# Kernel tuning notes

Hardware: AMD Instinct MI355X
Metric: run time of the kernel (lower is better)

## Reference

```python
import jax, jax.numpy as jnp
import numpy as np

N = 16000        # nodes
E = 256000       # edges
D_IN = 1280      # input node features
HID = 256        # hidden dim (all hidden_dims equal; required by res_linear shapes)
HEADS = 8
C = HID // HEADS # 32 channels per head
G = 32           # graphs in the batch
O = 64           # output labels (GO terms)
NB = 2           # conv blocks = len(hidden_dims) - 1
EPS = 1e-5


def _bn(h, g, b):
    # eval-mode BatchNorm1d with running_mean=0, running_var=1 (init state)
    return h * (g / jnp.sqrt(1.0 + EPS)) + b


def _seg_softmax(logits, seg, num):
    # numerically-stable segment softmax (PyG softmax semantics)
    m = jax.ops.segment_max(logits, seg, num_segments=num)
    e = jnp.exp(logits - m[seg])
    s = jax.ops.segment_sum(e, seg, num_segments=num)
    return e / (s[seg] + 1e-16)


def setup_inputs() -> dict:
    key = jax.random.key(0)
    ks = jax.random.split(key, 16)
    w = lambda i, sh: jax.random.normal(ks[i], sh, jnp.float32) * 0.05
    return {
        "x": jax.random.normal(ks[0], (N, D_IN), jnp.float32),
        "edge_index": jax.random.randint(ks[1], (2, E), 0, N),
        "batch": jnp.sort(jax.random.randint(ks[2], (N,), 0, G)),
        # feature_proj: Linear -> ReLU -> BN
        "fp_W": w(3, (D_IN, HID)), "fp_b": jnp.zeros(HID),
        "fp_g": jnp.ones(HID), "fp_be": jnp.zeros(HID),
        # GATv2Conv per block: lin_l, lin_r, att, out-bias
        "gat_Wl": w(4, (NB, HID, HID)), "gat_bl": jnp.zeros((NB, HID)),
        "gat_Wr": w(5, (NB, HID, HID)), "gat_br": jnp.zeros((NB, HID)),
        "gat_att": w(6, (NB, HEADS, C)), "gat_bias": jnp.zeros((NB, HID)),
        # GINConv MLP: Linear -> ReLU -> BN
        "gin_W": w(7, (NB, HID, HID)), "gin_b": jnp.zeros((NB, HID)),
        "gin_g": jnp.ones((NB, HID)), "gin_be": jnp.zeros((NB, HID)),
        # PyG LayerNorm (graph mode) affine
        "ln_g": jnp.ones((NB, HID)), "ln_b": jnp.zeros((NB, HID)),
        # residual linears
        "res_W": w(8, (NB, HID, HID)), "res_b": jnp.zeros((NB, HID)),
        # GlobalAttention gate MLP
        "pool_W1": w(9, (HID, HID)), "pool_b1": jnp.zeros(HID),
        "pool_W2": w(10, (HID, 1)), "pool_b2": jnp.zeros(1),
        # O label heads (hierarchy=None -> just the MLP), stacked
        "head_W1": w(11, (O, HID, 256)), "head_b1": jnp.zeros((O, 256)),
        "head_g": jnp.ones((O, 256)), "head_be": jnp.zeros((O, 256)),
        "head_W2": w(12, (O, 256)), "head_b2": jnp.zeros(O),
    }


def reference(x, edge_index, batch, fp_W, fp_b, fp_g, fp_be,
              gat_Wl, gat_bl, gat_Wr, gat_br, gat_att, gat_bias,
              gin_W, gin_b, gin_g, gin_be, ln_g, ln_b, res_W, res_b,
              pool_W1, pool_b1, pool_W2, pool_b2,
              head_W1, head_b1, head_g, head_be, head_W2, head_b2):
    n = x.shape[0]
    # feature_proj (eval: dropout = identity)
    h = _bn(jax.nn.relu(x @ fp_W + fp_b), fp_g, fp_be)

    src0, dst0 = edge_index[0], edge_index[1]
    loop = jnp.arange(n)
    src = jnp.concatenate([src0, loop])  # GATv2 adds self-loops by default
    dst = jnp.concatenate([dst0, loop])

    for i in range(NB):
        # ---- GATv2Conv (no activation after, per original control flow) ----
        xl = (h @ gat_Wl[i] + gat_bl[i]).reshape(n, HEADS, C)
        xr = (h @ gat_Wr[i] + gat_br[i]).reshape(n, HEADS, C)
        msg = xl[src]                                   # [E', H, C]
        eact = jax.nn.leaky_relu(msg + xr[dst], 0.2)
        logit = jnp.einsum('ehc,hc->eh', eact, gat_att[i])
        alpha = _seg_softmax(logit, dst, n)             # [E', H]
        h = jax.ops.segment_sum(alpha[:, :, None] * msg, dst,
                                num_segments=n).reshape(n, HID) + gat_bias[i]
        # ---- GINConv: nn((1+0)*x + sum_neighbors), then leaky_relu ----
        agg = jax.ops.segment_sum(h[src0], dst0, num_segments=n)
        gin = _bn(jax.nn.relu((h + agg) @ gin_W[i] + gin_b[i]), gin_g[i], gin_be[i])
        h = jax.nn.leaky_relu(gin, 0.2)
        # ---- PyG LayerNorm (graph mode, batch=None: global mean/std) + residual ----
        mu = h.mean()
        sd = jnp.std(h)
        ln = (h - mu) / (sd + EPS) * ln_g[i] + ln_b[i]
        h = jax.nn.leaky_relu(ln + (h @ res_W[i] + res_b[i]), 0.2)

    # ---- GlobalAttention pooling ----
    gate = jnp.tanh(h @ pool_W1 + pool_b1) @ pool_W2 + pool_b2   # [N, 1]
    a = _seg_softmax(gate[:, 0], batch, G)
    emb = jax.ops.segment_sum(a[:, None] * h, batch, num_segments=G)  # [G, HID]

    # ---- O label heads (hierarchy None -> MLP only), vectorized ----
    z = jnp.einsum('bd,odh->boh', emb, head_W1) + head_b1[None]
    z = _bn(jax.nn.silu(z), head_g[None], head_be[None])
    out = jnp.einsum('boh,oh->bo', z, head_W2) + head_b2[None]
    return out[:, :, None]  # torch.stack(outputs, dim=1) -> [G, O, 1]
```

## Files before the change

### kernel.cpp

```cpp
#include <hip/hip_runtime.h>
#include <math.h>

#define N_NODES 16000
#define N_EDGES 256000
#define EPE (N_EDGES + N_NODES)
#define DIN 1280
#define HID 256
#define HEADS 8
#define CPH 32
#define NG 32
#define NO 64
#define EPSC 1e-5f
#define CAP 32
#define XPAD 264
#define SPAD 40

typedef __bf16 bf16;
typedef __attribute__((ext_vector_type(8))) __bf16 bf16x8;
typedef __attribute__((ext_vector_type(4))) float floatx4;

__device__ __forceinline__ float lrelu(float v) { return v > 0.f ? v : 0.2f * v; }
__device__ __forceinline__ float bflo(unsigned int u) { return __uint_as_float(u << 16); }
__device__ __forceinline__ float bfhi(unsigned int u) { return __uint_as_float(u & 0xffff0000u); }
__device__ __forceinline__ unsigned int bfpack(float x, float y) {
    bf16 b0 = (bf16)x, b1 = (bf16)y;
    return ((unsigned int)*(unsigned short*)&b0) | (((unsigned int)*(unsigned short*)&b1) << 16);
}

__global__ void wconv_gen(const float* __restrict__ W, bf16* __restrict__ Wt, int K, int total) {
    int idx = blockIdx.x * 256 + threadIdx.x;
    if (idx >= total) return;
    int per = K * HID;
    int l = idx / per, rem = idx - l * per;
    int n = rem / K, k = rem - n * K;
    Wt[idx] = (bf16)W[(size_t)l * per + (size_t)k * HID + n];
}

__global__ void wconv_pair(const float* __restrict__ Wl, const float* __restrict__ Wr,
                           bf16* __restrict__ Wt) {
    int idx = blockIdx.x * 256 + threadIdx.x;
    int n = idx >> 8, k = idx & 255;
    float v = (n < 256) ? Wl[(size_t)k * HID + n] : Wr[(size_t)k * HID + (n - 256)];
    Wt[idx] = (bf16)v;
}

__global__ __launch_bounds__(256) void gemm64(
    const bf16* __restrict__ A, const bf16* __restrict__ Bt,
    const float* __restrict__ bias, const float* __restrict__ bias2,
    bf16* __restrict__ C, int K, int ldc, int mode,
    const float* __restrict__ g, const float* __restrict__ be,
    float2* __restrict__ statp, const float* __restrict__ stat)
{
    __shared__ __align__(16) bf16 As[2][64 * SPAD];
    __shared__ __align__(16) bf16 Bs[2][64 * SPAD];
    const int tid = threadIdx.x;
    const int bm = blockIdx.y * 64, bn = blockIdx.x * 64;
    const int w = tid >> 6, lane = tid & 63;
    const int wm = w * 16;
    const int lrow = lane & 15, lk8 = (lane >> 4) * 8;
    const int row = tid >> 2, k8 = (tid & 3) * 8;

    const bf16* gA = A + (size_t)(bm + row) * K + k8;
    const bf16* gB = Bt + (size_t)(bn + row) * K + k8;

    floatx4 acc[4];
#pragma unroll
    for (int j = 0; j < 4; j++) acc[j] = (floatx4){0.f, 0.f, 0.f, 0.f};

    const int nk = K >> 5;
    bf16x8 ra = *(const bf16x8*)gA;
    bf16x8 rb = *(const bf16x8*)gB;

    for (int it = 0; it < nk; ++it) {
        int p = it & 1;
        *(bf16x8*)&As[p][row * SPAD + k8] = ra;
        *(bf16x8*)&Bs[p][row * SPAD + k8] = rb;
        __syncthreads();
        if (it + 1 < nk) {
            ra = *(const bf16x8*)(gA + (it + 1) * 32);
            rb = *(const bf16x8*)(gB + (it + 1) * 32);
        }
        bf16x8 af = *(const bf16x8*)&As[p][(wm + lrow) * SPAD + lk8];
        bf16x8 bfr[4];
#pragma unroll
        for (int j = 0; j < 4; j++) bfr[j] = *(const bf16x8*)&Bs[p][(16 * j + lrow) * SPAD + lk8];
#pragma unroll
        for (int j = 0; j < 4; j++)
            acc[j] = __builtin_amdgcn_mfma_f32_16x16x32_bf16(af, bfr[j], acc[j], 0, 0, 0);
    }

    const float inv = rsqrtf(1.f + EPSC);
    const int row0 = bm + wm + (lane >> 4) * 4;
    float mu = 0.f, rs = 0.f;
    if (mode == 3) {
        const float inv_n = 1.f / (float)((size_t)N_NODES * HID);
        mu = stat[0] * inv_n;
        float var = stat[1] * inv_n - mu * mu;
        rs = 1.f / (sqrtf(fmaxf(var, 0.f)) + EPSC);
    }
    float sz = 0.f, sq = 0.f;
#pragma unroll
    for (int j = 0; j < 4; j++) {
        int col = bn + 16 * j + lrow;
        float bcol = (col < HID) ? bias[col] : bias2[col - HID];
        float gc = (mode >= 2) ? g[col] : 0.f;
        float bec = (mode >= 2) ? be[col] : 0.f;
#pragma unroll
        for (int r = 0; r < 4; r++) {
            float z = acc[j][r] + bcol;
            if (mode == 2) {
                z = fmaxf(z, 0.f) * (gc * inv) + bec;
                z = lrelu(z);
                sz += z; sq += z * z;
            } else if (mode == 3) {
                float h = (float)A[(size_t)(row0 + r) * K + col];
                z = (h - mu) * rs * gc + bec + z;
                z = lrelu(z);
            }
            C[(size_t)(row0 + r) * ldc + col] = (bf16)z;
        }
    }
    if (mode == 2) {
        for (int o = 32; o > 0; o >>= 1) { sz += __shfl_down(sz, o); sq += __shfl_down(sq, o); }
        __syncthreads();
        float* rs_ = (float*)&As[0][0];
        float* rq_ = (float*)&Bs[0][0];
        if (lane == 0) { rs_[w] = sz; rq_[w] = sq; }
        __syncthreads();
        if (tid == 0)
            statp[blockIdx.y * gridDim.x + blockIdx.x] =
                make_float2(rs_[0] + rs_[1] + rs_[2] + rs_[3],
                            rq_[0] + rq_[1] + rq_[2] + rq_[3]);
    }
}

__global__ __launch_bounds__(256, 1) void gemm_f32A(
    const float* __restrict__ A, const bf16* __restrict__ Bt,
    const float* __restrict__ bias, bf16* __restrict__ C, int K,
    const float* __restrict__ g, const float* __restrict__ be)
{
    __shared__ __align__(16) bf16 As[2][128 * SPAD];
    __shared__ __align__(16) bf16 Bs[2][128 * SPAD];
    const int tid = threadIdx.x;
    const int bm = blockIdx.y * 128, bn = blockIdx.x * 128;
    const int w = tid >> 6, lane = tid & 63;
    const int wm = (w & 1) * 64, wn = (w >> 1) * 64;
    const int lrow = lane & 15, lk8 = (lane >> 4) * 8;

    floatx4 acc[4][4];
#pragma unroll
    for (int i = 0; i < 4; i++)
#pragma unroll
        for (int j = 0; j < 4; j++) acc[i][j] = (floatx4){0.f, 0.f, 0.f, 0.f};

    const int r2 = tid >> 1, c2 = tid & 1;
    const float* gA = A + (size_t)(bm + r2) * K + c2 * 16;
    const bf16* gB = Bt + (size_t)(bn + r2) * K + c2 * 16;
    bf16* sA = &As[0][r2 * SPAD + c2 * 16];
    bf16* sB = &Bs[0][r2 * SPAD + c2 * 16];

    const int nk = K >> 5;
    float4 a[4][4];
    bf16x8 b[4][2];
#pragma unroll
    for (int u = 0; u < 4; u++) {
        const float* pa = gA + u * 32;
        a[u][0] = *(const float4*)(pa + 0);
        a[u][1] = *(const float4*)(pa + 4);
        a[u][2] = *(const float4*)(pa + 8);
        a[u][3] = *(const float4*)(pa + 12);
        const bf16* pb = gB + u * 32;
        b[u][0] = *(const bf16x8*)(pb + 0);
        b[u][1] = *(const bf16x8*)(pb + 8);
    }

    for (int it0 = 0; it0 < nk; it0 += 4) {
#pragma unroll
        for (int u = 0; u < 4; u++) {
            const int it = it0 + u;
            const int p = u & 1;
            const int po = p * 128 * SPAD;
            bf16x8 h0, h1;
            h0[0] = (bf16)a[u][0].x; h0[1] = (bf16)a[u][0].y; h0[2] = (bf16)a[u][0].z; h0[3] = (bf16)a[u][0].w;
            h0[4] = (bf16)a[u][1].x; h0[5] = (bf16)a[u][1].y; h0[6] = (bf16)a[u][1].z; h0[7] = (bf16)a[u][1].w;
            h1[0] = (bf16)a[u][2].x; h1[1] = (bf16)a[u][2].y; h1[2] = (bf16)a[u][2].z; h1[3] = (bf16)a[u][2].w;
            h1[4] = (bf16)a[u][3].x; h1[5] = (bf16)a[u][3].y; h1[6] = (bf16)a[u][3].z; h1[7] = (bf16)a[u][3].w;
            *(bf16x8*)(sA + po + 0) = h0;
            *(bf16x8*)(sA + po + 8) = h1;
            *(bf16x8*)(sB + po + 0) = b[u][0];
            *(bf16x8*)(sB + po + 8) = b[u][1];
            __syncthreads();
            if (it + 4 < nk) {
                const float* pa = gA + (it + 4) * 32;
                a[u][0] = *(const float4*)(pa + 0);
                a[u][1] = *(const float4*)(pa + 4);
                a[u][2] = *(const float4*)(pa + 8);
                a[u][3] = *(const float4*)(pa + 12);
                const bf16* pb = gB + (it + 4) * 32;
                b[u][0] = *(const bf16x8*)(pb + 0);
                b[u][1] = *(const bf16x8*)(pb + 8);
            }
            bf16x8 af[4], bfr[4];
#pragma unroll
            for (int i = 0; i < 4; i++) af[i] = *(const bf16x8*)&As[p][(wm + 16 * i + lrow) * SPAD + lk8];
#pragma unroll
            for (int j = 0; j < 4; j++) bfr[j] = *(const bf16x8*)&Bs[p][(wn + 16 * j + lrow) * SPAD + lk8];
#pragma unroll
            for (int i = 0; i < 4; i++)
#pragma unroll
                for (int j = 0; j < 4; j++)
                    acc[i][j] = __builtin_amdgcn_mfma_f32_16x16x32_bf16(af[i], bfr[j], acc[i][j], 0, 0, 0);
        }
    }

    const float inv = rsqrtf(1.f + EPSC);
#pragma unroll
    for (int j = 0; j < 4; j++) {
        int col = bn + wn + 16 * j + lrow;
        float bcol = bias[col];
        float gc = g[col] * inv;
        float bec = be[col];
#pragma unroll
        for (int i = 0; i < 4; i++) {
            int row0 = bm + wm + 16 * i + (lane >> 4) * 4;
#pragma unroll
            for (int r = 0; r < 4; r++) {
                float z = fmaxf(acc[i][j][r] + bcol, 0.f) * gc + bec;
                C[(size_t)(row0 + r) * HID + col] = (bf16)z;
            }
        }
    }
}

__global__ void hist_kernel(const int* __restrict__ ei, int* __restrict__ cnt) {
    int e = blockIdx.x * 256 + threadIdx.x;
    if (e >= EPE) return;
    int d = (e < N_EDGES) ? ei[N_EDGES + e] : (e - N_EDGES);
    atomicAdd(&cnt[d], 1);
}

__global__ __launch_bounds__(1024) void scan_kernel(const int* __restrict__ cnt,
                                                    int* __restrict__ roff, int* __restrict__ cursor,
                                                    const int* __restrict__ batch,
                                                    int* __restrict__ gstart) {
    __shared__ int wsum[16];
    int t = threadIdx.x;
    int base = t * 16;
    int local[16]; int s = 0;
#pragma unroll
    for (int i = 0; i < 16; i++) {
        int idx = base + i;
        int v = (idx < N_NODES) ? cnt[idx] : 0;
        local[i] = s; s += v;
    }
    int lane = t & 63, wid = t >> 6;
    int incl = s;
    for (int o = 1; o < 64; o <<= 1) { int v = __shfl_up(incl, o); if (lane >= o) incl += v; }
    if (lane == 63) wsum[wid] = incl;
    __syncthreads();
    if (t == 0) { int a = 0; for (int k = 0; k < 16; k++) { int v = wsum[k]; wsum[k] = a; a += v; } }
    __syncthreads();
    int texcl = incl - s + wsum[wid];
#pragma unroll
    for (int i = 0; i < 16; i++) {
        int idx = base + i;
        if (idx < N_NODES) { int o = texcl + local[i]; roff[idx] = o; cursor[idx] = o; }
    }
    if (t == 1023) roff[N_NODES] = texcl + s;
    if (t <= NG) {
        int lo = 0, hi = N_NODES;
        while (lo < hi) { int mid = (lo + hi) >> 1; if (batch[mid] < t) lo = mid + 1; else hi = mid; }
        gstart[t] = lo;
    }
}

__global__ void scatter_kernel(const int* __restrict__ ei, int* __restrict__ cursor,
                               int* __restrict__ esrc) {
    int e = blockIdx.x * 256 + threadIdx.x;
    if (e >= EPE) return;
    int s, d;
    if (e < N_EDGES) { s = ei[e]; d = ei[N_EDGES + e]; }
    else { s = d = e - N_EDGES; }
    int pos = atomicAdd(&cursor[d], 1);
    esrc[pos] = s;
}

__global__ __launch_bounds__(256) void gat_fused(
    const bf16* __restrict__ XLR, const int* __restrict__ roff, const int* __restrict__ esrc,
    const float* __restrict__ att, const float* __restrict__ gbias, bf16* __restrict__ out)
{
    const int d = blockIdx.x, t = threadIdx.x;
    const int beg = roff[d], deg = roff[d + 1] - beg;
    __shared__ __align__(16) bf16 xs[CAP][XPAD];
    __shared__ __align__(16) float4 xa4[8 * 16];
    __shared__ float llog[CAP * 8];
    __shared__ float comb[256];
    __shared__ float m_s[8], s_s[8], resc[8];

    if (t < 128) {
        int hh = t >> 4, cc = t & 15;
        int c = hh * 32 + cc * 2;
        float xr0 = (float)XLR[(size_t)d * 512 + 256 + c];
        float xr1 = (float)XLR[(size_t)d * 512 + 256 + c + 1];
        xa4[hh * 16 + cc] = (float4){xr0, att[c], xr1, att[c + 1]};
    }
    if (t < 8) { m_s[t] = -INFINITY; s_s[t] = 0.f; }

    const int jj = t & 31;
    const int hh = t >> 5;
    const int sg = t >> 5, sl = t & 31;
    const int half = t >> 7;
    const int tc = t & 127;
    const int ch0 = tc * 2;
    const int ha = tc >> 4;
    float a0 = 0.f, a1 = 0.f;

    for (int c0 = 0; c0 < deg; c0 += CAP) {
        int cn = min(CAP, deg - c0);
        __syncthreads();
        for (int r = sg; r < cn; r += 8) {
            int s = esrc[beg + c0 + r];
            *(bf16x8*)(&xs[r][sl * 8]) = *(const bf16x8*)(XLR + (size_t)s * 512 + sl * 8);
        }
        __syncthreads();
        if (jj < cn) {
            float lg = 0.f;
#pragma unroll
            for (int cc = 0; cc < 16; cc++) {
                int ce = (cc + jj) & 15;
                unsigned int p = *(const unsigned int*)&xs[jj][hh * 32 + ce * 2];
                float4 xa = xa4[hh * 16 + ce];
                lg += lrelu(bflo(p) + xa.x) * xa.y + lrelu(bfhi(p) + xa.z) * xa.w;
            }
            llog[jj * 8 + hh] = lg;
        }
        __syncthreads();
        if (t < 64) {
            int h2 = t & 7, j0 = t >> 3;
            float mx = -INFINITY;
            for (int j = j0; j < cn; j += 8) mx = fmaxf(mx, llog[j * 8 + h2]);
            for (int o = 8; o < 64; o <<= 1) mx = fmaxf(mx, __shfl_xor(mx, o));
            float mo = m_s[h2];
            float mn = fmaxf(mo, mx);
            float ss = 0.f;
            for (int j = j0; j < cn; j += 8) {
                float e = __expf(llog[j * 8 + h2] - mn);
                llog[j * 8 + h2] = e;
                ss += e;
            }
            for (int o = 8; o < 64; o <<= 1) ss += __shfl_xor(ss, o);
            if (t < 8) {
                float r = __expf(mo - mn);
                resc[h2] = r;
                s_s[h2] = s_s[h2] * r + ss;
                m_s[h2] = mn;
            }
        }
        __syncthreads();
        float rsf = resc[ha];
        a0 *= rsf; a1 *= rsf;
        for (int j = half; j < cn; j += 2) {
            float wgt = llog[j * 8 + ha];
            unsigned int p = *(const unsigned int*)&xs[j][ch0];
            a0 = fmaf(wgt, bflo(p), a0);
            a1 = fmaf(wgt, bfhi(p), a1);
        }
    }
    __syncthreads();
    if (half) { comb[ch0] = a0; comb[ch0 + 1] = a1; }
    __syncthreads();
    if (!half) {
        float r = 1.f / (s_s[ha] + 1e-16f);
        float v0 = gbias[ch0] + (a0 + comb[ch0]) * r;
        float v1 = gbias[ch0 + 1] + (a1 + comb[ch0 + 1]) * r;
        *(unsigned int*)(out + (size_t)d * HID + ch0) = bfpack(v0, v1);
    }
}

__global__ __launch_bounds__(256) void gin_gather(
    const unsigned int* __restrict__ hu, const int* __restrict__ roff,
    const int* __restrict__ esrc, unsigned int* __restrict__ uu)
{
    int d = blockIdx.x, t = threadIdx.x;
    int grp = t >> 7, c = t & 127;
    int beg = roff[d], end = roff[d + 1];
    float a0 = 0.f, a1 = 0.f;
    int p = beg + grp;
    while (p + 14 < end) {
        int s[8];
#pragma unroll
        for (int k = 0; k < 8; k++) s[k] = esrc[p + 2 * k];
        unsigned int v[8];
#pragma unroll
        for (int k = 0; k < 8; k++) v[k] = hu[(size_t)s[k] * 128 + c];
#pragma unroll
        for (int k = 0; k < 8; k++) { a0 += bflo(v[k]); a1 += bfhi(v[k]); }
        p += 16;
    }
    for (; p < end; p += 2) {
        unsigned int v = hu[(size_t)esrc[p] * 128 + c];
        a0 += bflo(v); a1 += bfhi(v);
    }
    __shared__ float plo[128], phi[128];
    if (grp) { plo[c] = a0; phi[c] = a1; }
    __syncthreads();
    if (!grp) {
        a0 += plo[c]; a1 += phi[c];
        uu[(size_t)d * 128 + c] = bfpack(a0, a1);
    }
}

__global__ void stats_reduce(const float2* __restrict__ part, float* __restrict__ stat, int n) {
    int t = threadIdx.x;
    float s = 0.f, q = 0.f;
    for (int i = t; i < n; i += 256) { float2 v = part[i]; s += v.x; q += v.y; }
    for (int o = 32; o > 0; o >>= 1) { s += __shfl_down(s, o); q += __shfl_down(q, o); }
    __shared__ float ls[4], lq[4];
    int wid = t >> 6, lane = t & 63;
    if (lane == 0) { ls[wid] = s; lq[wid] = q; }
    __syncthreads();
    if (t == 0) { stat[0] = ls[0] + ls[1] + ls[2] + ls[3]; stat[1] = lq[0] + lq[1] + lq[2] + lq[3]; }
}

__global__ __launch_bounds__(256) void pool_gate_kernel(const bf16* __restrict__ t,
    const float* __restrict__ W2, const float* __restrict__ b2, float* __restrict__ gate)
{
    int n = blockIdx.x * 4 + (threadIdx.x >> 6);
    int lane = threadIdx.x & 63;
    const bf16* p = t + (size_t)n * HID + lane * 4;
    float4 w = *(const float4*)(W2 + lane * 4);
    float s = tanhf((float)p[0]) * w.x + tanhf((float)p[1]) * w.y
            + tanhf((float)p[2]) * w.z + tanhf((float)p[3]) * w.w;
    for (int o = 32; o > 0; o >>= 1) s += __shfl_down(s, o);
    if (lane == 0) gate[n] = s + b2[0];
}

__global__ __launch_bounds__(256) void pool_stats_kernel(
    float* __restrict__ gate, const int* __restrict__ gstart)
{
    int g = blockIdx.x, t = threadIdx.x;
    int lo = gstart[g], hi = gstart[g + 1];
    __shared__ float red[256];
    float m = -INFINITY;
    for (int n = lo + t; n < hi; n += 256) m = fmaxf(m, gate[n]);
    red[t] = m; __syncthreads();
    for (int st = 128; st > 0; st >>= 1) { if (t < st) red[t] = fmaxf(red[t], red[t + st]); __syncthreads(); }
    m = red[0]; __syncthreads();
    float s = 0.f;
    for (int n = lo + t; n < hi; n += 256) s += __expf(gate[n] - m);
    red[t] = s; __syncthreads();
    for (int st = 128; st > 0; st >>= 1) { if (t < st) red[t] += red[t + st]; __syncthreads(); }
    float sinv = 1.f / (red[0] + 1e-16f);
    for (int n = lo + t; n < hi; n += 256) gate[n] = __expf(gate[n] - m) * sinv;
}

__global__ __launch_bounds__(256) void emb_accum_kernel(
    const float* __restrict__ a, const int* __restrict__ batch,
    const bf16* __restrict__ h, float* __restrict__ emb)
{
    int n0 = blockIdx.x * 32, t = threadIdx.x;
    int cur = batch[n0]; float acc = 0.f;
    for (int j = 0; j < 32; j++) {
        int n = n0 + j;
        int b = batch[n];
        if (b != cur) { atomicAdd(&emb[cur * HID + t], acc); cur = b; acc = 0.f; }
        acc += a[n] * (float)h[(size_t)n * HID + t];
    }
    atomicAdd(&emb[cur * HID + t], acc);
}

__global__ __launch_bounds__(256) void heads_kernel(
    const float* __restrict__ emb, const float* __restrict__ W1, const float* __restrict__ b1,
    const float* __restrict__ hg, const float* __restrict__ hbe, const float* __restrict__ W2,
    const float* __restrict__ b2, float* __restrict__ out)
{
    int o = blockIdx.x;
    int g0 = blockIdx.y * 4;
    int k = threadIdx.x;
    __shared__ float se[4][HID];
    __shared__ float red[256];
#pragma unroll
    for (int j = 0; j < 4; j++) se[j][k] = emb[(g0 + j) * HID + k];
    __syncthreads();
    const float* w1p = W1 + (size_t)o * HID * HID + k;
    float zb = b1[o * HID + k];
    float z0 = zb, z1 = zb, z2 = zb, z3 = zb;
#pragma unroll 8
    for (int d = 0; d < HID; d++) {
        float w = w1p[(size_t)d * HID];
        z0 = fmaf(se[0][d], w, z0);
        z1 = fmaf(se[1][d], w, z1);
        z2 = fmaf(se[2][d], w, z2);
        z3 = fmaf(se[3][d], w, z3);
    }
    const float gk = hg[o * HID + k] * rsqrtf(1.f + EPSC);
    const float bek = hbe[o * HID + k];
    const float w2 = W2[o * HID + k];
    const float b2o = b2[o];
    float zz[4] = {z0, z1, z2, z3};
#pragma unroll
    for (int j = 0; j < 4; j++) {
        float z = zz[j];
        float sil = z / (1.f + expf(-z));
        red[k] = (sil * gk + bek) * w2;
        __syncthreads();
        for (int st = 128; st > 0; st >>= 1) { if (k < st) red[k] += red[k + st]; __syncthreads(); }
        if (k == 0) out[(g0 + j) * NO + o] = red[0] + b2o;
        __syncthreads();
    }
}

extern "C" void kernel_launch(void* const* d_in, const int* in_sizes, int n_in,
                              void* d_out, int out_size, void* d_ws, size_t ws_size,
                              hipStream_t stream) {
    const float* x        = (const float*)d_in[0];
    const int*   ei       = (const int*)  d_in[1];
    const int*   batch    = (const int*)  d_in[2];
    const float* fp_W     = (const float*)d_in[3];
    const float* fp_b     = (const float*)d_in[4];
    const float* fp_g     = (const float*)d_in[5];
    const float* fp_be    = (const float*)d_in[6];
    const float* gat_Wl   = (const float*)d_in[7];
    const float* gat_bl   = (const float*)d_in[8];
    const float* gat_Wr   = (const float*)d_in[9];
    const float* gat_br   = (const float*)d_in[10];
    const float* gat_att  = (const float*)d_in[11];
    const float* gat_bias = (const float*)d_in[12];
    const float* gin_W    = (const float*)d_in[13];
    const float* gin_b    = (const float*)d_in[14];
    const float* gin_g    = (const float*)d_in[15];
    const float* gin_be   = (const float*)d_in[16];
    const float* ln_g     = (const float*)d_in[17];
    const float* ln_b     = (const float*)d_in[18];
    const float* res_W    = (const float*)d_in[19];
    const float* res_b    = (const float*)d_in[20];
    const float* pool_W1  = (const float*)d_in[21];
    const float* pool_b1  = (const float*)d_in[22];
    const float* pool_W2  = (const float*)d_in[23];
    const float* pool_b2  = (const float*)d_in[24];
    const float* head_W1  = (const float*)d_in[25];
    const float* head_b1  = (const float*)d_in[26];
    const float* head_g   = (const float*)d_in[27];
    const float* head_be  = (const float*)d_in[28];
    const float* head_W2  = (const float*)d_in[29];
    const float* head_b2  = (const float*)d_in[30];
    float* out = (float*)d_out;

    char* base = (char*)d_ws;
    size_t off = 0;
    auto alloc = [&](size_t bytes) -> char* {
        char* p = base + off; off += (bytes + 255) & ~(size_t)255; return p;
    };
    int*   esrc   = (int*)  alloc((size_t)EPE * 4);
    int*   cnt    = (int*)  alloc((size_t)N_NODES * 4);
    int*   roff   = (int*)  alloc((size_t)(N_NODES + 1) * 4);
    int*   cursor = (int*)  alloc((size_t)N_NODES * 4);
    float* gate   = (float*)alloc((size_t)N_NODES * 4);
    int*   gstart = (int*)  alloc((NG + 1) * 4);
    float* emb    = (float*)alloc(NG * HID * 4);
    float* stat   = (float*)alloc(8);
    float2* statp = (float2*)alloc(1024 * 8);
    bf16*  Hb0    = (bf16*) alloc((size_t)N_NODES * HID * 2);
    bf16*  Hb1    = (bf16*) alloc((size_t)N_NODES * HID * 2);
    bf16*  XLR    = (bf16*) alloc((size_t)N_NODES * 512 * 2);
    bf16*  fpWt   = (bf16*) alloc((size_t)DIN * HID * 2);
    bf16*  wlrT0  = (bf16*) alloc((size_t)512 * HID * 2);
    bf16*  wlrT1  = (bf16*) alloc((size_t)512 * HID * 2);
    bf16*  gwT    = (bf16*) alloc((size_t)2 * HID * HID * 2);
    bf16*  rwT    = (bf16*) alloc((size_t)2 * HID * HID * 2);
    bf16*  pwT    = (bf16*) alloc((size_t)HID * HID * 2);
    bf16*  Ub     = XLR;
    bf16*  wlrT[2] = { wlrT0, wlrT1 };

    wconv_gen<<<(DIN * HID + 255) / 256, 256, 0, stream>>>(fp_W, fpWt, DIN, DIN * HID);
    wconv_pair<<<512, 256, 0, stream>>>(gat_Wl, gat_Wr, wlrT0);
    wconv_pair<<<512, 256, 0, stream>>>(gat_Wl + HID * HID, gat_Wr + HID * HID, wlrT1);
    wconv_gen<<<512, 256, 0, stream>>>(gin_W, gwT, HID, 2 * HID * HID);
    wconv_gen<<<512, 256, 0, stream>>>(res_W, rwT, HID, 2 * HID * HID);
    wconv_gen<<<256, 256, 0, stream>>>(pool_W1, pwT, HID, HID * HID);

    hipMemsetAsync(cnt, 0, N_NODES * sizeof(int), stream);
    hist_kernel<<<(EPE + 255) / 256, 256, 0, stream>>>(ei, cnt);
    scan_kernel<<<1, 1024, 0, stream>>>(cnt, roff, cursor, batch, gstart);
    scatter_kernel<<<(EPE + 255) / 256, 256, 0, stream>>>(ei, cursor, esrc);

    dim3 gridF(2, 125);
    dim3 g64_256(4, 250);
    dim3 g64_512(8, 250);
    gemm_f32A<<<gridF, 256, 0, stream>>>(x, fpWt, fp_b, Hb0, DIN, fp_g, fp_be);

    bf16* hcur = Hb0;
    bf16* hoth = Hb1;
    for (int i = 0; i < 2; i++) {
        gemm64<<<g64_512, 256, 0, stream>>>(hcur, wlrT[i], gat_bl + i * HID, gat_br + i * HID,
                                            XLR, HID, 512, 0, nullptr, nullptr, nullptr, nullptr);
        gat_fused<<<N_NODES, 256, 0, stream>>>(XLR, roff, esrc, gat_att + i * HEADS * CPH,
                                               gat_bias + i * HID, hoth);
        gin_gather<<<N_NODES, 256, 0, stream>>>((const unsigned int*)hoth, roff, esrc,
                                                (unsigned int*)Ub);
        gemm64<<<g64_256, 256, 0, stream>>>(Ub, gwT + (size_t)i * HID * HID, gin_b + i * HID,
                                            nullptr, hcur, HID, HID, 2,
                                            gin_g + i * HID, gin_be + i * HID, statp, nullptr);
        stats_reduce<<<1, 256, 0, stream>>>(statp, stat, 1000);
        gemm64<<<g64_256, 256, 0, stream>>>(hcur, rwT + (size_t)i * HID * HID, res_b + i * HID,
                                            nullptr, hoth, HID, HID, 3,
                                            ln_g + i * HID, ln_b + i * HID, nullptr, stat);
        bf16* tmp = hcur; hcur = hoth; hoth = tmp;
    }

    gemm64<<<g64_256, 256, 0, stream>>>(hcur, pwT, pool_b1, nullptr, hoth, HID, HID, 0,
                                        nullptr, nullptr, nullptr, nullptr);
    pool_gate_kernel<<<N_NODES / 4, 256, 0, stream>>>(hoth, pool_W2, pool_b2, gate);
    pool_stats_kernel<<<NG, 256, 0, stream>>>(gate, gstart);
    hipMemsetAsync(emb, 0, NG * HID * sizeof(float), stream);
    emb_accum_kernel<<<N_NODES / 32, 256, 0, stream>>>(gate, batch, hcur, emb);

    dim3 hgrid(NO, 8);
    heads_kernel<<<hgrid, 256, 0, stream>>>(emb, head_W1, head_b1, head_g, head_be,
                                            head_W2, head_b2, out);
}
```

Measured before the change: 595.7 us.

## Map one wavefront per node in GAT and GIN edge aggregation kernels

Replaces the block-per-node GAT kernel, which staged neighbor rows in shared memory and synchronized several times per chunk, with a wavefront-per-node kernel using an online softmax. Each lane handles 4 channels, head logits are reduced with 8-lane shuffles, and the next edge's row is prefetched. The GIN gather likewise becomes one wave per node with 2-edge unrolling. This removes shared memory and barriers but serializes each node's edges within a single wave, which limits memory-level parallelism per node.

```diff
diff --git a/kernel.cpp b/kernel.cpp
--- a/kernel.cpp
+++ b/kernel.cpp
@@ -11,8 +11,6 @@
 #define NG 32
 #define NO 64
 #define EPSC 1e-5f
-#define CAP 32
-#define XPAD 264
 #define SPAD 40
 
 typedef __bf16 bf16;
@@ -285,129 +283,94 @@
     esrc[pos] = s;
 }
 
-__global__ __launch_bounds__(256) void gat_fused(
+__global__ __launch_bounds__(256) void gat_wave(
     const bf16* __restrict__ XLR, const int* __restrict__ roff, const int* __restrict__ esrc,
     const float* __restrict__ att, const float* __restrict__ gbias, bf16* __restrict__ out)
 {
-    const int d = blockIdx.x, t = threadIdx.x;
-    const int beg = roff[d], deg = roff[d + 1] - beg;
-    __shared__ __align__(16) bf16 xs[CAP][XPAD];
-    __shared__ __align__(16) float4 xa4[8 * 16];
-    __shared__ float llog[CAP * 8];
-    __shared__ float comb[256];
-    __shared__ float m_s[8], s_s[8], resc[8];
-
-    if (t < 128) {
-        int hh = t >> 4, cc = t & 15;
-        int c = hh * 32 + cc * 2;
-        float xr0 = (float)XLR[(size_t)d * 512 + 256 + c];
-        float xr1 = (float)XLR[(size_t)d * 512 + 256 + c + 1];
-        xa4[hh * 16 + cc] = (float4){xr0, att[c], xr1, att[c + 1]};
-    }
-    if (t < 8) { m_s[t] = -INFINITY; s_s[t] = 0.f; }
-
-    const int jj = t & 31;
-    const int hh = t >> 5;
-    const int sg = t >> 5, sl = t & 31;
-    const int half = t >> 7;
-    const int tc = t & 127;
-    const int ch0 = tc * 2;
-    const int ha = tc >> 4;
-    float a0 = 0.f, a1 = 0.f;
-
-    for (int c0 = 0; c0 < deg; c0 += CAP) {
-        int cn = min(CAP, deg - c0);
-        __syncthreads();
-        for (int r = sg; r < cn; r += 8) {
-            int s = esrc[beg + c0 + r];
-            *(bf16x8*)(&xs[r][sl * 8]) = *(const bf16x8*)(XLR + (size_t)s * 512 + sl * 8);
+    const int wid = threadIdx.x >> 6;
+    const int lane = threadIdx.x & 63;
+    const int d = blockIdx.x * 4 + wid;
+    const int beg = roff[d], end = roff[d + 1];
+    const int c0 = lane * 4;
+
+    const unsigned int* xru = (const unsigned int*)(XLR + (size_t)d * 512 + 256 + c0);
+    const unsigned int xr01 = xru[0], xr23 = xru[1];
+    const float xr0 = bflo(xr01), xr1 = bfhi(xr01), xr2 = bflo(xr23), xr3 = bfhi(xr23);
+    const float at0 = att[c0], at1 = att[c0 + 1], at2 = att[c0 + 2], at3 = att[c0 + 3];
+
+    float m = -INFINITY, s = 0.f;
+    float a0 = 0.f, a1 = 0.f, a2 = 0.f, a3 = 0.f;
+
+    int src = esrc[beg];
+    const unsigned int* xp = (const unsigned int*)(XLR + (size_t)src * 512 + c0);
+    unsigned int xl01 = xp[0], xl23 = xp[1];
+
+    for (int e = beg; e < end; ++e) {
+        unsigned int nx01 = 0u, nx23 = 0u;
+        if (e + 1 < end) {
+            int ns = esrc[e + 1];
+            const unsigned int* np = (const unsigned int*)(XLR + (size_t)ns * 512 + c0);
+            nx01 = np[0]; nx23 = np[1];
         }
-        __syncthreads();
-        if (jj < cn) {
-            float lg = 0.f;
-#pragma unroll
-            for (int cc = 0; cc < 16; cc++) {
-                int ce = (cc + jj) & 15;
-                unsigned int p = *(const unsigned int*)&xs[jj][hh * 32 + ce * 2];
-                float4 xa = xa4[hh * 16 + ce];
-                lg += lrelu(bflo(p) + xa.x) * xa.y + lrelu(bfhi(p) + xa.z) * xa.w;
-            }
-            llog[jj * 8 + hh] = lg;
-        }
-        __syncthreads();
-        if (t < 64) {
-            int h2 = t & 7, j0 = t >> 3;
-            float mx = -INFINITY;
-            for (int j = j0; j < cn; j += 8) mx = fmaxf(mx, llog[j * 8 + h2]);
-            for (int o = 8; o < 64; o <<= 1) mx = fmaxf(mx, __shfl_xor(mx, o));
-            float mo = m_s[h2];
-            float mn = fmaxf(mo, mx);
-            float ss = 0.f;
-            for (int j = j0; j < cn; j += 8) {
-                float e = __expf(llog[j * 8 + h2] - mn);
-                llog[j * 8 + h2] = e;
-                ss += e;
-            }
-            for (int o = 8; o < 64; o <<= 1) ss += __shfl_xor(ss, o);
-            if (t < 8) {
-                float r = __expf(mo - mn);
-                resc[h2] = r;
-                s_s[h2] = s_s[h2] * r + ss;
-                m_s[h2] = mn;
-            }
-        }
-        __syncthreads();
-        float rsf = resc[ha];
-        a0 *= rsf; a1 *= rsf;
-        for (int j = half; j < cn; j += 2) {
-            float wgt = llog[j * 8 + ha];
-            unsigned int p = *(const unsigned int*)&xs[j][ch0];
-            a0 = fmaf(wgt, bflo(p), a0);
-            a1 = fmaf(wgt, bfhi(p), a1);
-        }
-    }
-    __syncthreads();
-    if (half) { comb[ch0] = a0; comb[ch0 + 1] = a1; }
-    __syncthreads();
-    if (!half) {
-        float r = 1.f / (s_s[ha] + 1e-16f);
-        float v0 = gbias[ch0] + (a0 + comb[ch0]) * r;
-        float v1 = gbias[ch0 + 1] + (a1 + comb[ch0 + 1]) * r;
-        *(unsigned int*)(out + (size_t)d * HID + ch0) = bfpack(v0, v1);
-    }
-}
-
-__global__ __launch_bounds__(256) void gin_gather(
-    const unsigned int* __restrict__ hu, const int* __restrict__ roff,
-    const int* __restrict__ esrc, unsigned int* __restrict__ uu)
-{
-    int d = blockIdx.x, t = threadIdx.x;
-    int grp = t >> 7, c = t & 127;
-    int beg = roff[d], end = roff[d + 1];
-    float a0 = 0.f, a1 = 0.f;
-    int p = beg + grp;
-    while (p + 14 < end) {
-        int s[8];
-#pragma unroll
-        for (int k = 0; k < 8; k++) s[k] = esrc[p + 2 * k];
-        unsigned int v[8];
-#pragma unroll
-        for (int k = 0; k < 8; k++) v[k] = hu[(size_t)s[k] * 128 + c];
-#pragma unroll
-        for (int k = 0; k < 8; k++) { a0 += bflo(v[k]); a1 += bfhi(v[k]); }
-        p += 16;
-    }
-    for (; p < end; p += 2) {
-        unsigned int v = hu[(size_t)esrc[p] * 128 + c];
-        a0 += bflo(v); a1 += bfhi(v);
-    }
-    __shared__ float plo[128], phi[128];
-    if (grp) { plo[c] = a0; phi[c] = a1; }
-    __syncthreads();
-    if (!grp) {
-        a0 += plo[c]; a1 += phi[c];
-        uu[(size_t)d * 128 + c] = bfpack(a0, a1);
-    }
+        float x0 = bflo(xl01), x1 = bfhi(xl01), x2 = bflo(xl23), x3 = bfhi(xl23);
+        float p = lrelu(x0 + xr0) * at0 + lrelu(x1 + xr1) * at1
+                + lrelu(x2 + xr2) * at2 + lrelu(x3 + xr3) * at3;
+        p += __shfl_xor(p, 1);
+        p += __shfl_xor(p, 2);
+        p += __shfl_xor(p, 4);
+        float mn = fmaxf(m, p);
+        float rsc = __expf(m - mn);
+        float wgt = __expf(p - mn);
+        s = s * rsc + wgt;
+        a0 = a0 * rsc + wgt * x0;
+        a1 = a1 * rsc + wgt * x1;
+        a2 = a2 * rsc + wgt * x2;
+        a3 = a3 * rsc + wgt * x3;
+        m = mn;
+        xl01 = nx01; xl23 = nx23;
+    }
+
+    const float rinv = 1.f / (s + 1e-16f);
+    float v0 = gbias[c0]     + a0 * rinv;
+    float v1 = gbias[c0 + 1] + a1 * rinv;
+    float v2 = gbias[c0 + 2] + a2 * rinv;
+    float v3 = gbias[c0 + 3] + a3 * rinv;
+    unsigned int* op = (unsigned int*)(out + (size_t)d * HID + c0);
+    op[0] = bfpack(v0, v1);
+    op[1] = bfpack(v2, v3);
+}
+
+__global__ __launch_bounds__(256) void gin_wave(
+    const bf16* __restrict__ H, const int* __restrict__ roff,
+    const int* __restrict__ esrc, bf16* __restrict__ U)
+{
+    const int wid = threadIdx.x >> 6;
+    const int lane = threadIdx.x & 63;
+    const int d = blockIdx.x * 4 + wid;
+    const int beg = roff[d], end = roff[d + 1];
+    const int c0 = lane * 4;
+
+    float a0 = 0.f, a1 = 0.f, a2 = 0.f, a3 = 0.f;
+    int e = beg;
+    for (; e + 1 < end; e += 2) {
+        int s0 = esrc[e], s1 = esrc[e + 1];
+        const unsigned int* p0 = (const unsigned int*)(H + (size_t)s0 * HID + c0);
+        const unsigned int* p1 = (const unsigned int*)(H + (size_t)s1 * HID + c0);
+        unsigned int u01 = p0[0], u23 = p0[1];
+        unsigned int v01 = p1[0], v23 = p1[1];
+        a0 += bflo(u01) + bflo(v01);
+        a1 += bfhi(u01) + bfhi(v01);
+        a2 += bflo(u23) + bflo(v23);
+        a3 += bfhi(u23) + bfhi(v23);
+    }
+    if (e < end) {
+        const unsigned int* p0 = (const unsigned int*)(H + (size_t)esrc[e] * HID + c0);
+        unsigned int u01 = p0[0], u23 = p0[1];
+        a0 += bflo(u01); a1 += bfhi(u01); a2 += bflo(u23); a3 += bfhi(u23);
+    }
+    unsigned int* up = (unsigned int*)(U + (size_t)d * HID + c0);
+    up[0] = bfpack(a0, a1);
+    up[1] = bfpack(a2, a3);
 }
 
 __global__ void stats_reduce(const float2* __restrict__ part, float* __restrict__ stat, int n) {
@@ -594,10 +557,9 @@
     for (int i = 0; i < 2; i++) {
         gemm64<<<g64_512, 256, 0, stream>>>(hcur, wlrT[i], gat_bl + i * HID, gat_br + i * HID,
                                             XLR, HID, 512, 0, nullptr, nullptr, nullptr, nullptr);
-        gat_fused<<<N_NODES, 256, 0, stream>>>(XLR, roff, esrc, gat_att + i * HEADS * CPH,
-                                               gat_bias + i * HID, hoth);
-        gin_gather<<<N_NODES, 256, 0, stream>>>((const unsigned int*)hoth, roff, esrc,
-                                                (unsigned int*)Ub);
+        gat_wave<<<N_NODES / 4, 256, 0, stream>>>(XLR, roff, esrc, gat_att + i * HEADS * CPH,
+                                                  gat_bias + i * HID, hoth);
+        gin_wave<<<N_NODES / 4, 256, 0, stream>>>(hoth, roff, esrc, Ub);
         gemm64<<<g64_256, 256, 0, stream>>>(Ub, gwT + (size_t)i * HID * HID, gin_b + i * HID,
                                             nullptr, hcur, HID, HID, 2,
                                             gin_g + i * HID, gin_be + i * HID, statp, nullptr);
```

New measurement: 562.0 us. 1.06x faster.
